# Performance work log

Measured on AMD Instinct MI355X. Metric: run time of the kernel, lower is better.

The kernel has to match this reference:

```python
import jax, jax.numpy as jnp
import numpy as np

B, T, C = 4, 4096, 1024
H = 16          # n_head
LS = 256        # local block size (block-causal window)
EPS = 1e-6


def rmsnorm(x, w):
    # matches RMSNorm: x * rsqrt(mean(x^2) + eps) * weight, computed in fp32
    xf = x.astype(jnp.float32)
    y = xf * jax.lax.rsqrt(jnp.mean(xf * xf, axis=-1, keepdims=True) + EPS)
    return y.astype(x.dtype) * w


def setup_inputs() -> dict:
    key = jax.random.key(0)
    k1, k2, k3 = jax.random.split(key, 3)
    x = jax.random.normal(k1, (B, T, C), dtype=jnp.float32)
    w_qkv = jax.random.normal(k2, (C, 3 * C), dtype=jnp.float32) * (1.0 / np.sqrt(C))
    ln_w = jnp.ones((C,), dtype=jnp.float32)
    w_proj = jax.random.normal(k3, (C, C), dtype=jnp.float32) * (1.0 / np.sqrt(C))
    return {"x": x, "w_qkv": w_qkv, "ln_w": ln_w, "w_proj": w_proj}


def reference(x, w_qkv, ln_w, w_proj):
    Bx, Tx, Cx = x.shape
    ng = Tx // LS                      # number of causal blocks
    hd = Cx // H                       # head dim
    # group tokens into blocks: [B, ng, ls, C]
    xg = x.reshape(Bx, ng, LS, Cx)
    qkv = jnp.einsum('bglc,cd->bgld', xg, w_qkv)
    q, k, v = jnp.split(qkv, 3, axis=-1)
    # fused QK RMSNorm over full embed dim (before head split), shared weight
    q = rmsnorm(q, ln_w)
    k = rmsnorm(k, ln_w)
    # split heads: [B, ng, H, ls, hd]
    q = q.reshape(Bx, ng, LS, H, hd).transpose(0, 1, 3, 2, 4)
    k = k.reshape(Bx, ng, LS, H, hd).transpose(0, 1, 3, 2, 4)
    v = v.reshape(Bx, ng, LS, H, hd).transpose(0, 1, 3, 2, 4)
    scale = 1.0 / np.sqrt(hd)          # muP=False
    att = jnp.einsum('bghqd,bghkd->bghqk', q, k) * scale
    causal = jnp.tril(jnp.ones((LS, LS), dtype=bool))
    att = jnp.where(causal, att, -jnp.finfo(att.dtype).max)
    att = jax.nn.softmax(att, axis=-1)
    y = jnp.einsum('bghqk,bghkd->bghqd', att, v)
    # merge heads and blocks back: [B, T, C]
    y = y.transpose(0, 1, 3, 2, 4).reshape(Bx, Tx, Cx)
    return jnp.einsum('btc,cd->btd', y, w_proj)
```

## Files before the change

### kernel.cpp

```cpp
#include <hip/hip_runtime.h>

typedef __attribute__((ext_vector_type(4))) float f32x4;
typedef __attribute__((ext_vector_type(8))) short bf16x8;
typedef __attribute__((ext_vector_type(4))) unsigned short u16x4;
typedef __attribute__((ext_vector_type(8))) unsigned short u16x8;
typedef unsigned short u16;
typedef unsigned int u32;

#define M_  16384
#define C_  1024
#define N1_ 3072

__device__ __forceinline__ float bf2f(u16 u) {
  union { u32 i; float f; } v; v.i = ((u32)u) << 16; return v.f;
}
__device__ __forceinline__ u16 f2bf(float f) {
  union { float f; u32 i; } v; v.f = f;
  u32 r = v.i + 0x7fffu + ((v.i >> 16) & 1u);
  return (u16)(r >> 16);
}

__device__ __forceinline__ void gload16(const void* g, void* l) {
  __builtin_amdgcn_global_load_lds(
      (const __attribute__((address_space(1))) u32*)g,
      (__attribute__((address_space(3))) u32*)l, 16, 0, 0);
}

__global__ __launch_bounds__(256) void cast_f32_bf16(const float* __restrict__ in,
                                                     u16* __restrict__ out) {
  size_t i = (size_t)blockIdx.x * 256 + threadIdx.x;
  f32x4 v = ((const f32x4*)in)[i];
  u16x4 o = { f2bf(v[0]), f2bf(v[1]), f2bf(v[2]), f2bf(v[3]) };
  ((u16x4*)out)[i] = o;
}

__global__ __launch_bounds__(256) void transpose_cast(const float* __restrict__ in,
                                                      u16* __restrict__ out, int K, int N) {
  __shared__ u16 tile[64][65];
  const int n0 = blockIdx.x * 64, k0 = blockIdx.y * 64;
  const int tid = threadIdx.x;
  const int nn = tid & 63, kk = tid >> 6;
#pragma unroll
  for (int r = 0; r < 16; ++r)
    tile[kk * 16 + r][nn] = f2bf(in[(size_t)(k0 + kk * 16 + r) * N + n0 + nn]);
  __syncthreads();
  const int kc = tid & 15, nl = tid >> 4;
#pragma unroll
  for (int p = 0; p < 4; ++p) {
    const int n = p * 16 + nl;
    u16x4 v = { tile[kc * 4 + 0][n], tile[kc * 4 + 1][n],
                tile[kc * 4 + 2][n], tile[kc * 4 + 3][n] };
    *(u16x4*)(out + (size_t)(n0 + n) * K + k0 + kc * 4) = v;
  }
}

__device__ __forceinline__ void store16(float* dst, f32x4 v0, f32x4 v1, f32x4 v2, f32x4 v3) {
  ((f32x4*)dst)[0] = v0; ((f32x4*)dst)[1] = v1; ((f32x4*)dst)[2] = v2; ((f32x4*)dst)[3] = v3;
}
__device__ __forceinline__ void store16(u16* dst, f32x4 v0, f32x4 v1, f32x4 v2, f32x4 v3) {
  u16x8 o0 = { f2bf(v0[0]), f2bf(v0[1]), f2bf(v0[2]), f2bf(v0[3]),
               f2bf(v1[0]), f2bf(v1[1]), f2bf(v1[2]), f2bf(v1[3]) };
  u16x8 o1 = { f2bf(v2[0]), f2bf(v2[1]), f2bf(v2[2]), f2bf(v2[3]),
               f2bf(v3[0]), f2bf(v3[1]), f2bf(v3[2]), f2bf(v3[3]) };
  *(u16x8*)dst = o0; *(u16x8*)(dst + 8) = o1;
}

template <typename OUT>
__global__ __launch_bounds__(512, 2) void gemm256(const u16* __restrict__ A,
                                                  const u16* __restrict__ BT,
                                                  OUT* __restrict__ C,
                                                  int M, int N, int ntn) {
  constexpr int KC = 1024;
  __shared__ __align__(16) u16 sA0[256 * 64], sA1[256 * 64];
  __shared__ __align__(16) u16 sB0[256 * 64], sB1[256 * 64];
  const int tid = threadIdx.x, lane = tid & 63, w = tid >> 6;
  const int wm = w >> 2, wn = w & 3;

  int bid = blockIdx.x;
  const int cpx = gridDim.x >> 3;
  bid = (bid & 7) * cpx + (bid >> 3);
  const int tm = (bid / ntn) << 8, tn = (bid % ntn) << 8;

  const u16* srcA[4]; const u16* srcB[4]; int ldsOff[4];
#pragma unroll
  for (int l = 0; l < 4; ++l) {
    const int g = l * 512 + tid;
    const int row = g >> 3, c = g & 7;
    srcA[l] = A + (size_t)(tm + row) * KC + ((c ^ (row & 7)) << 3);
    srcB[l] = BT + (size_t)(tn + row) * KC + ((c ^ (row & 7)) << 3);
    ldsOff[l] = g << 4;
  }

#define STAGE(sa, sb, kt) do { const int _k0 = (kt) << 6;                      \
    _Pragma("unroll") for (int _l = 0; _l < 4; ++_l) {                         \
      gload16(srcA[_l] + _k0, (char*)(sa) + ldsOff[_l]);                       \
      gload16(srcB[_l] + _k0, (char*)(sb) + ldsOff[_l]); } } while (0)

  const int swz = (lane & 7) << 4;
  const int r16 = lane & 15;
  const int kb = (lane >> 4) << 4;
#define LDA_(sa, fm, ks) (*(const bf16x8*)((const char*)(sa) + \
    (wm * 128 + (fm) * 16 + r16) * 128 + ((((ks) << 6) | kb) ^ swz)))
#define LDB_(sb, fn, ks) (*(const bf16x8*)((const char*)(sb) + \
    (wn * 64 + (fn) * 16 + r16) * 128 + ((((ks) << 6) | kb) ^ swz)))

  f32x4 acc[8][4];
#pragma unroll
  for (int i = 0; i < 8; ++i)
#pragma unroll
    for (int j = 0; j < 4; ++j) acc[i][j] = (f32x4){0.f, 0.f, 0.f, 0.f};

#define MM(i, j, a_, b_) acc[i][j] = __builtin_amdgcn_mfma_f32_16x16x32_bf16(a_, b_, acc[i][j], 0, 0, 0)

#define KTILE(sa, sb, ...) do {                                                \
  bf16x8 ka[4][2], kb0[2][2], kb1[2][2];                                       \
  _Pragma("unroll") for (int fm = 0; fm < 4; ++fm) {                           \
    ka[fm][0] = LDA_(sa, fm, 0); ka[fm][1] = LDA_(sa, fm, 1); }                \
  _Pragma("unroll") for (int fn = 0; fn < 2; ++fn) {                           \
    kb0[fn][0] = LDB_(sb, fn, 0); kb0[fn][1] = LDB_(sb, fn, 1); }              \
  __builtin_amdgcn_s_barrier();                                                \
  __builtin_amdgcn_s_setprio(1);                                               \
  _Pragma("unroll") for (int fm = 0; fm < 4; ++fm)                             \
    _Pragma("unroll") for (int fn = 0; fn < 2; ++fn) {                         \
      MM(fm, fn, ka[fm][0], kb0[fn][0]); MM(fm, fn, ka[fm][1], kb0[fn][1]); }  \
  __builtin_amdgcn_s_setprio(0);                                               \
  __builtin_amdgcn_s_barrier();                                                \
  _Pragma("unroll") for (int fn = 0; fn < 2; ++fn) {                           \
    kb1[fn][0] = LDB_(sb, 2 + fn, 0); kb1[fn][1] = LDB_(sb, 2 + fn, 1); }      \
  __builtin_amdgcn_s_barrier();                                                \
  __builtin_amdgcn_s_setprio(1);                                               \
  _Pragma("unroll") for (int fm = 0; fm < 4; ++fm)                             \
    _Pragma("unroll") for (int fn = 0; fn < 2; ++fn) {                         \
      MM(fm, 2 + fn, ka[fm][0], kb1[fn][0]); MM(fm, 2 + fn, ka[fm][1], kb1[fn][1]); } \
  __builtin_amdgcn_s_setprio(0);                                               \
  __builtin_amdgcn_s_barrier();                                                \
  _Pragma("unroll") for (int fm = 0; fm < 4; ++fm) {                           \
    ka[fm][0] = LDA_(sa, 4 + fm, 0); ka[fm][1] = LDA_(sa, 4 + fm, 1); }        \
  __builtin_amdgcn_s_barrier();                                                \
  __builtin_amdgcn_s_setprio(1);                                               \
  _Pragma("unroll") for (int fm = 0; fm < 4; ++fm)                             \
    _Pragma("unroll") for (int fn = 0; fn < 2; ++fn) {                         \
      MM(4 + fm, 2 + fn, ka[fm][0], kb1[fn][0]); MM(4 + fm, 2 + fn, ka[fm][1], kb1[fn][1]); } \
  __builtin_amdgcn_s_setprio(0);                                               \
  __builtin_amdgcn_s_barrier();                                                \
  __builtin_amdgcn_sched_barrier(0);                                           \
  __VA_ARGS__;                                                                 \
  __builtin_amdgcn_s_setprio(1);                                               \
  _Pragma("unroll") for (int fm = 0; fm < 4; ++fm)                             \
    _Pragma("unroll") for (int fn = 0; fn < 2; ++fn) {                         \
      MM(4 + fm, fn, ka[fm][0], kb0[fn][0]); MM(4 + fm, fn, ka[fm][1], kb0[fn][1]); } \
  __builtin_amdgcn_s_setprio(0);                                               \
} while (0)

#define TILE_ENTRY(vm) do { __builtin_amdgcn_sched_barrier(0);                 \
    asm volatile("s_waitcnt vmcnt(" #vm ")");                                  \
    __builtin_amdgcn_sched_barrier(0);                                         \
    __builtin_amdgcn_s_barrier();                                              \
    __builtin_amdgcn_sched_barrier(0); } while (0)

  STAGE(sA0, sB0, 0);
  STAGE(sA1, sB1, 1);

#pragma unroll 1
  for (int i = 0; i < 7; ++i) {
    TILE_ENTRY(8);
    KTILE(sA0, sB0, STAGE(sA0, sB0, 2 * i + 2));
    TILE_ENTRY(8);
    KTILE(sA1, sB1, STAGE(sA1, sB1, 2 * i + 3));
  }
  TILE_ENTRY(8);
  KTILE(sA0, sB0, (void)0);
  TILE_ENTRY(0);
  KTILE(sA1, sB1, (void)0);

  __syncthreads();
  u16* eb = (w == 0) ? sA0 : (w == 1) ? sA0 + 8192 : (w == 2) ? sA1 : (w == 3) ? sA1 + 8192
          : (w == 4) ? sB0 : (w == 5) ? sB0 + 8192 : (w == 6) ? sB1 : sB1 + 8192;
  float* fb = (float*)eb;
  const int erow = lane >> 2, eseg = lane & 3;
#pragma unroll
  for (int fm = 0; fm < 8; ++fm) {
#pragma unroll
    for (int fn = 0; fn < 4; ++fn)
#pragma unroll
      for (int r = 0; r < 4; ++r)
        fb[((lane >> 4) * 4 + r) * 68 + fn * 16 + (lane & 15)] = acc[fm][fn][r];
    asm volatile("s_waitcnt lgkmcnt(0)" ::: "memory");
    const float* src = &fb[erow * 68 + eseg * 16];
    f32x4 v0 = ((const f32x4*)src)[0], v1 = ((const f32x4*)src)[1];
    f32x4 v2 = ((const f32x4*)src)[2], v3 = ((const f32x4*)src)[3];
    OUT* dst = C + (size_t)(tm + wm * 128 + fm * 16 + erow) * N + tn + wn * 64 + eseg * 16;
    store16(dst, v0, v1, v2, v3);
  }
#undef STAGE
#undef LDA_
#undef LDB_
#undef MM
#undef KTILE
#undef TILE_ENTRY
}

__global__ __launch_bounds__(256) void qk_scales(const u16* __restrict__ qkv,
                                                 float* __restrict__ qscl,
                                                 float* __restrict__ kscl) {
  const int t = blockIdx.x * 4 + (threadIdx.x >> 6);
  const int lane = threadIdx.x & 63;
  const u16* row = qkv + (size_t)t * N1_;
#pragma unroll
  for (int part = 0; part < 2; ++part) {
    const u16* p = row + part * C_ + lane * 16;
    bf16x8 v0 = *(const bf16x8*)p;
    bf16x8 v1 = *(const bf16x8*)(p + 8);
    float ss = 0.f;
#pragma unroll
    for (int e = 0; e < 8; ++e) {
      float a = bf2f((u16)v0[e]), b = bf2f((u16)v1[e]);
      ss += a * a + b * b;
    }
#pragma unroll
    for (int o = 1; o < 64; o <<= 1) ss += __shfl_xor(ss, o, 64);
    if (lane == 0) {
      float s = rsqrtf(ss * (1.0f / 1024.0f) + 1e-6f);
      (part ? kscl : qscl)[t] = s;
    }
  }
}

__global__ __launch_bounds__(256, 1) void attn_kernel(const u16* __restrict__ qkv,
                                                      const float* __restrict__ qscl,
                                                      const float* __restrict__ kscl,
                                                      const float* __restrict__ lnw,
                                                      u16* __restrict__ y) {
  const int bid = blockIdx.x;
  const int h = bid & 15;
  const int bg = bid >> 4;
  const size_t rowbase = (size_t)bg * 256;
  const u16* Qg = qkv + rowbase * N1_ + h * 64;
  const u16* Kg = Qg + C_;
  const u16* Vg = Qg + 2 * C_;

  __shared__ __align__(16) u16 Ks[256 * 64];
  __shared__ __align__(16) u16 Vt[64 * 256];
  __shared__ __align__(16) u16 Ps[4][16 * 256];

  const int tid = threadIdx.x;
  const int lane = tid & 63;
  const int w = tid >> 6;
  const int g = lane >> 4;
  const int qi = lane & 15;

  {
    const int r = tid;
    const u16* kr = Kg + (size_t)r * N1_;
    const u16* vr = Vg + (size_t)r * N1_;
    const float ksc = kscl[rowbase + r];
    const float* lw = lnw + h * 64;
    char* ksb = (char*)Ks + r * 128;
    const int swk = (r & 7) << 4;
#pragma unroll
    for (int j = 0; j < 8; ++j) {
      bf16x8 kv = *(const bf16x8*)(kr + j * 8);
      f32x4 wa = *(const f32x4*)(lw + j * 8);
      f32x4 wb = *(const f32x4*)(lw + j * 8 + 4);
#pragma unroll
      for (int e = 0; e < 4; ++e) {
        kv[e]     = (short)f2bf(bf2f((u16)kv[e]) * ksc * wa[e]);
        kv[4 + e] = (short)f2bf(bf2f((u16)kv[4 + e]) * ksc * wb[e]);
      }
      *(bf16x8*)(ksb + ((j * 16) ^ swk)) = kv;
      bf16x8 vv = *(const bf16x8*)(vr + j * 8);
#pragma unroll
      for (int e = 0; e < 8; ++e) {
        int d = j * 8 + e;
        *(u16*)((char*)Vt + d * 512 + ((2 * r) ^ ((d & 7) << 4))) = (u16)vv[e];
      }
    }
  }
  float lnq0[8], lnq1[8];
#pragma unroll
  for (int e = 0; e < 8; ++e) {
    lnq0[e] = lnw[h * 64 + g * 8 + e];
    lnq1[e] = lnw[h * 64 + 32 + g * 8 + e];
  }
  __syncthreads();

  const float scale = 0.125f;
  char* pb = (char*)Ps[w];
  const int swq = (qi & 7) << 4;

#pragma unroll 1
  for (int j = 0; j < 4; ++j) {
    const int qt = ((j >> 1) << 3) + ((j & 1) ? (7 - w) : w);

    const u16* qrow = Qg + (size_t)(qt * 16 + qi) * N1_ + g * 8;
    const float qsc = qscl[rowbase + qt * 16 + qi];
    bf16x8 q0 = *(const bf16x8*)(qrow);
    bf16x8 q1 = *(const bf16x8*)(qrow + 32);
#pragma unroll
    for (int e = 0; e < 8; ++e) {
      q0[e] = (short)f2bf(bf2f((u16)q0[e]) * qsc * lnq0[e]);
      q1[e] = (short)f2bf(bf2f((u16)q1[e]) * qsc * lnq1[e]);
    }

    f32x4 s[16];
#pragma unroll
    for (int n = 0; n < 16; ++n) {
      if (n <= qt) {
        const char* kb = (const char*)Ks + (n * 16 + qi) * 128;
        bf16x8 ka0 = *(const bf16x8*)(kb + ((g * 16) ^ swq));
        bf16x8 ka1 = *(const bf16x8*)(kb + ((g * 16 + 64) ^ swq));
        f32x4 a = {0.f, 0.f, 0.f, 0.f};
        a = __builtin_amdgcn_mfma_f32_16x16x32_bf16(ka0, q0, a, 0, 0, 0);
        a = __builtin_amdgcn_mfma_f32_16x16x32_bf16(ka1, q1, a, 0, 0, 0);
        s[n] = a;
      }
    }

    const int q_abs = qt * 16 + qi;
    float m = -3e38f;
#pragma unroll
    for (int n = 0; n < 16; ++n) if (n <= qt) {
#pragma unroll
      for (int r = 0; r < 4; ++r) {
        const int k_abs = n * 16 + g * 4 + r;
        float v = s[n][r] * scale;
        v = (k_abs <= q_abs) ? v : -3e38f;
        s[n][r] = v;
        m = fmaxf(m, v);
      }
    }
    m = fmaxf(m, __shfl_xor(m, 16, 64));
    m = fmaxf(m, __shfl_xor(m, 32, 64));

    float sum = 0.f;
#pragma unroll
    for (int n = 0; n < 16; ++n) if (n <= qt) {
#pragma unroll
      for (int r = 0; r < 4; ++r) {
        float p = __expf(s[n][r] - m);
        s[n][r] = p;
        sum += p;
      }
    }
    sum += __shfl_xor(sum, 16, 64);
    sum += __shfl_xor(sum, 32, 64);

#pragma unroll
    for (int n = 0; n < 16; ++n) if (n <= qt) {
      u16x4 pk = { f2bf(s[n][0]), f2bf(s[n][1]), f2bf(s[n][2]), f2bf(s[n][3]) };
      *(u16x4*)(pb + qi * 512 + ((n * 32 + g * 8) ^ swq)) = pk;
    }
    if (!(qt & 1)) {
      u16x4 z = {0, 0, 0, 0};
      *(u16x4*)(pb + qi * 512 + (((qt + 1) * 32 + g * 8) ^ swq)) = z;
    }

    f32x4 yacc[4];
#pragma unroll
    for (int dn = 0; dn < 4; ++dn) yacc[dn] = (f32x4){0.f, 0.f, 0.f, 0.f};
    const int nkf = qt / 2 + 1;
#pragma unroll
    for (int kf = 0; kf < 8; ++kf) if (kf < nkf) {
      bf16x8 pa = *(const bf16x8*)(pb + qi * 512 + ((kf * 64 + g * 16) ^ swq));
#pragma unroll
      for (int dn = 0; dn < 4; ++dn) {
        const int d = dn * 16 + qi;
        bf16x8 vb = *(const bf16x8*)((const char*)Vt + d * 512 + ((kf * 64 + g * 16) ^ swq));
        yacc[dn] = __builtin_amdgcn_mfma_f32_16x16x32_bf16(pa, vb, yacc[dn], 0, 0, 0);
      }
    }

#pragma unroll
    for (int r = 0; r < 4; ++r) {
      const float inv = 1.0f / __shfl(sum, g * 4 + r, 64);
      const size_t trow = rowbase + (size_t)qt * 16 + g * 4 + r;
      u16* yrow = y + trow * C_ + h * 64 + qi;
#pragma unroll
      for (int dn = 0; dn < 4; ++dn) yrow[dn * 16] = f2bf(yacc[dn][r] * inv);
    }
  }
}

extern "C" void kernel_launch(void* const* d_in, const int* in_sizes, int n_in,
                              void* d_out, int out_size, void* d_ws, size_t ws_size,
                              hipStream_t stream) {
  const float* x      = (const float*)d_in[0];
  const float* w_qkv  = (const float*)d_in[1];
  const float* ln_w   = (const float*)d_in[2];
  const float* w_proj = (const float*)d_in[3];
  float* out = (float*)d_out;

  u16* xb     = (u16*)d_ws;
  u16* wqkvT  = xb + (size_t)M_ * C_;
  u16* wprojT = wqkvT + (size_t)N1_ * C_;
  u16* qkvb   = wprojT + (size_t)C_ * C_;
  u16* yb     = qkvb + (size_t)M_ * N1_;
  float* qscl = (float*)(yb + (size_t)M_ * C_);
  float* kscl = qscl + M_;

  cast_f32_bf16<<<(M_ * C_) / 1024, 256, 0, stream>>>(x, xb);
  transpose_cast<<<dim3(N1_ / 64, C_ / 64), 256, 0, stream>>>(w_qkv, wqkvT, C_, N1_);
  transpose_cast<<<dim3(C_ / 64, C_ / 64), 256, 0, stream>>>(w_proj, wprojT, C_, C_);

  gemm256<u16><<<(M_ / 256) * (N1_ / 256), 512, 0, stream>>>(xb, wqkvT, qkvb, M_, N1_, N1_ / 256);
  qk_scales<<<M_ / 4, 256, 0, stream>>>(qkvb, qscl, kscl);
  attn_kernel<<<64 * 16, 256, 0, stream>>>(qkvb, qscl, kscl, ln_w, yb);
  gemm256<float><<<(M_ / 256) * (C_ / 256), 512, 0, stream>>>(yb, wprojT, out, M_, C_, C_ / 256);
}
```

Before: 293.7 us.

## Fuse QK sum-of-squares into QKV GEMM epilogue and store per-head blocked layout

```diff
diff --git a/kernel.cpp b/kernel.cpp
--- a/kernel.cpp
+++ b/kernel.cpp
@@ -10,6 +10,7 @@
 #define M_  16384
 #define C_  1024
 #define N1_ 3072
+#define PSZ ((size_t)M_ * 64 * 16 / 16 * 4 / 4)
 
 __device__ __forceinline__ float bf2f(u16 u) {
   union { u32 i; float f; } v; v.i = ((u32)u) << 16; return v.f;
@@ -69,10 +70,13 @@
 __global__ __launch_bounds__(512, 2) void gemm256(const u16* __restrict__ A,
                                                   const u16* __restrict__ BT,
                                                   OUT* __restrict__ C,
-                                                  int M, int N, int ntn) {
+                                                  int M, int N, int ntn,
+                                                  float* __restrict__ ssq,
+                                                  float* __restrict__ ssk) {
   constexpr int KC = 1024;
   __shared__ __align__(16) u16 sA0[256 * 64], sA1[256 * 64];
   __shared__ __align__(16) u16 sB0[256 * 64], sB1[256 * 64];
+  __shared__ float ssred[4][256];
   const int tid = threadIdx.x, lane = tid & 63, w = tid >> 6;
   const int wm = w >> 2, wn = w & 3;
 
@@ -174,10 +178,40 @@
   KTILE(sA1, sB1, (void)0);
 
   __syncthreads();
+
+  const int part = tn >> 10;
+  const int cp = tn & 1023;
+  const int bg = tm >> 8;
+  const int hh = (cp >> 6) + wn;
+  if constexpr (sizeof(OUT) == 2) {
+    if (part < 2) {
+#pragma unroll
+      for (int fm = 0; fm < 8; ++fm)
+#pragma unroll
+        for (int r = 0; r < 4; ++r) {
+          float s = acc[fm][0][r] * acc[fm][0][r] + acc[fm][1][r] * acc[fm][1][r]
+                  + acc[fm][2][r] * acc[fm][2][r] + acc[fm][3][r] * acc[fm][3][r];
+          s += __shfl_xor(s, 1, 64); s += __shfl_xor(s, 2, 64);
+          s += __shfl_xor(s, 4, 64); s += __shfl_xor(s, 8, 64);
+          if (r16 == 0) ssred[wn][wm * 128 + fm * 16 + (lane >> 4) * 4 + r] = s;
+        }
+      __syncthreads();
+      if (tid < 256) {
+        float s = ssred[0][tid] + ssred[1][tid] + ssred[2][tid] + ssred[3][tid];
+        (part == 0 ? ssq : ssk)[(size_t)(tm + tid) * 4 + (cp >> 8)] = s;
+      }
+    }
+  }
+
   u16* eb = (w == 0) ? sA0 : (w == 1) ? sA0 + 8192 : (w == 2) ? sA1 : (w == 3) ? sA1 + 8192
           : (w == 4) ? sB0 : (w == 5) ? sB0 + 8192 : (w == 6) ? sB1 : sB1 + 8192;
   float* fb = (float*)eb;
   const int erow = lane >> 2, eseg = lane & 3;
+  OUT* dstb;
+  if constexpr (sizeof(OUT) == 2)
+    dstb = C + (size_t)part * ((size_t)M_ * C_) + ((size_t)(bg * 16 + hh) * 256) * 64;
+  else
+    dstb = C + (size_t)(tm) * N + tn + wn * 64;
 #pragma unroll
   for (int fm = 0; fm < 8; ++fm) {
 #pragma unroll
@@ -189,7 +223,11 @@
     const float* src = &fb[erow * 68 + eseg * 16];
     f32x4 v0 = ((const f32x4*)src)[0], v1 = ((const f32x4*)src)[1];
     f32x4 v2 = ((const f32x4*)src)[2], v3 = ((const f32x4*)src)[3];
-    OUT* dst = C + (size_t)(tm + wm * 128 + fm * 16 + erow) * N + tn + wn * 64 + eseg * 16;
+    OUT* dst;
+    if constexpr (sizeof(OUT) == 2)
+      dst = dstb + (size_t)(wm * 128 + fm * 16 + erow) * 64 + eseg * 16;
+    else
+      dst = dstb + (size_t)(wm * 128 + fm * 16 + erow) * N + eseg * 16;
     store16(dst, v0, v1, v2, v3);
   }
 #undef STAGE
@@ -200,48 +238,22 @@
 #undef TILE_ENTRY
 }
 
-__global__ __launch_bounds__(256) void qk_scales(const u16* __restrict__ qkv,
-                                                 float* __restrict__ qscl,
-                                                 float* __restrict__ kscl) {
-  const int t = blockIdx.x * 4 + (threadIdx.x >> 6);
-  const int lane = threadIdx.x & 63;
-  const u16* row = qkv + (size_t)t * N1_;
-#pragma unroll
-  for (int part = 0; part < 2; ++part) {
-    const u16* p = row + part * C_ + lane * 16;
-    bf16x8 v0 = *(const bf16x8*)p;
-    bf16x8 v1 = *(const bf16x8*)(p + 8);
-    float ss = 0.f;
-#pragma unroll
-    for (int e = 0; e < 8; ++e) {
-      float a = bf2f((u16)v0[e]), b = bf2f((u16)v1[e]);
-      ss += a * a + b * b;
-    }
-#pragma unroll
-    for (int o = 1; o < 64; o <<= 1) ss += __shfl_xor(ss, o, 64);
-    if (lane == 0) {
-      float s = rsqrtf(ss * (1.0f / 1024.0f) + 1e-6f);
-      (part ? kscl : qscl)[t] = s;
-    }
-  }
-}
-
-__global__ __launch_bounds__(256, 1) void attn_kernel(const u16* __restrict__ qkv,
-                                                      const float* __restrict__ qscl,
-                                                      const float* __restrict__ kscl,
+__global__ __launch_bounds__(256, 2) void attn_kernel(const u16* __restrict__ qkvblk,
+                                                      const float* __restrict__ ssq,
+                                                      const float* __restrict__ ssk,
                                                       const float* __restrict__ lnw,
                                                       u16* __restrict__ y) {
   const int bid = blockIdx.x;
   const int h = bid & 15;
   const int bg = bid >> 4;
   const size_t rowbase = (size_t)bg * 256;
-  const u16* Qg = qkv + rowbase * N1_ + h * 64;
-  const u16* Kg = Qg + C_;
-  const u16* Vg = Qg + 2 * C_;
-
-  __shared__ __align__(16) u16 Ks[256 * 64];
+  const u16* Qb = qkvblk + ((size_t)(bg * 16 + h) * 256) * 64;
+  const u16* Kb = Qb + (size_t)M_ * C_;
+  const u16* Vb = Qb + 2 * (size_t)M_ * C_;
+
   __shared__ __align__(16) u16 Vt[64 * 256];
   __shared__ __align__(16) u16 Ps[4][16 * 256];
+  __shared__ float kscl[256];
 
   const int tid = threadIdx.x;
   const int lane = tid & 63;
@@ -251,23 +263,9 @@
 
   {
     const int r = tid;
-    const u16* kr = Kg + (size_t)r * N1_;
-    const u16* vr = Vg + (size_t)r * N1_;
-    const float ksc = kscl[rowbase + r];
-    const float* lw = lnw + h * 64;
-    char* ksb = (char*)Ks + r * 128;
-    const int swk = (r & 7) << 4;
+    const u16* vr = Vb + (size_t)r * 64;
 #pragma unroll
     for (int j = 0; j < 8; ++j) {
-      bf16x8 kv = *(const bf16x8*)(kr + j * 8);
-      f32x4 wa = *(const f32x4*)(lw + j * 8);
-      f32x4 wb = *(const f32x4*)(lw + j * 8 + 4);
-#pragma unroll
-      for (int e = 0; e < 4; ++e) {
-        kv[e]     = (short)f2bf(bf2f((u16)kv[e]) * ksc * wa[e]);
-        kv[4 + e] = (short)f2bf(bf2f((u16)kv[4 + e]) * ksc * wb[e]);
-      }
-      *(bf16x8*)(ksb + ((j * 16) ^ swk)) = kv;
       bf16x8 vv = *(const bf16x8*)(vr + j * 8);
 #pragma unroll
       for (int e = 0; e < 8; ++e) {
@@ -275,25 +273,29 @@
         *(u16*)((char*)Vt + d * 512 + ((2 * r) ^ ((d & 7) << 4))) = (u16)vv[e];
       }
     }
+    f32x4 kp = ((const f32x4*)ssk)[rowbase + r];
+    kscl[r] = rsqrtf((kp[0] + kp[1] + kp[2] + kp[3]) * (1.0f / 1024.0f) + 1e-6f);
   }
   float lnq0[8], lnq1[8];
 #pragma unroll
   for (int e = 0; e < 8; ++e) {
-    lnq0[e] = lnw[h * 64 + g * 8 + e];
-    lnq1[e] = lnw[h * 64 + 32 + g * 8 + e];
+    float a = lnw[h * 64 + g * 8 + e];
+    float b = lnw[h * 64 + 32 + g * 8 + e];
+    lnq0[e] = a * a; lnq1[e] = b * b;
   }
   __syncthreads();
 
-  const float scale = 0.125f;
   char* pb = (char*)Ps[w];
   const int swq = (qi & 7) << 4;
 
 #pragma unroll 1
   for (int j = 0; j < 4; ++j) {
     const int qt = ((j >> 1) << 3) + ((j & 1) ? (7 - w) : w);
-
-    const u16* qrow = Qg + (size_t)(qt * 16 + qi) * N1_ + g * 8;
-    const float qsc = qscl[rowbase + qt * 16 + qi];
+    const int q = qt * 16 + qi;
+
+    f32x4 qv = ((const f32x4*)ssq)[rowbase + q];
+    const float qsc = rsqrtf((qv[0] + qv[1] + qv[2] + qv[3]) * (1.0f / 1024.0f) + 1e-6f);
+    const u16* qrow = Qb + (size_t)q * 64 + g * 8;
     bf16x8 q0 = *(const bf16x8*)(qrow);
     bf16x8 q1 = *(const bf16x8*)(qrow + 32);
 #pragma unroll
@@ -306,9 +308,9 @@
 #pragma unroll
     for (int n = 0; n < 16; ++n) {
       if (n <= qt) {
-        const char* kb = (const char*)Ks + (n * 16 + qi) * 128;
-        bf16x8 ka0 = *(const bf16x8*)(kb + ((g * 16) ^ swq));
-        bf16x8 ka1 = *(const bf16x8*)(kb + ((g * 16 + 64) ^ swq));
+        const u16* krow = Kb + (size_t)(n * 16 + qi) * 64 + g * 8;
+        bf16x8 ka0 = *(const bf16x8*)(krow);
+        bf16x8 ka1 = *(const bf16x8*)(krow + 32);
         f32x4 a = {0.f, 0.f, 0.f, 0.f};
         a = __builtin_amdgcn_mfma_f32_16x16x32_bf16(ka0, q0, a, 0, 0, 0);
         a = __builtin_amdgcn_mfma_f32_16x16x32_bf16(ka1, q1, a, 0, 0, 0);
@@ -316,15 +318,15 @@
       }
     }
 
-    const int q_abs = qt * 16 + qi;
     float m = -3e38f;
 #pragma unroll
     for (int n = 0; n < 16; ++n) if (n <= qt) {
+      f32x4 k4 = *(const f32x4*)&kscl[n * 16 + g * 4];
 #pragma unroll
       for (int r = 0; r < 4; ++r) {
         const int k_abs = n * 16 + g * 4 + r;
-        float v = s[n][r] * scale;
-        v = (k_abs <= q_abs) ? v : -3e38f;
+        float v = s[n][r] * 0.125f * k4[r];
+        v = (k_abs <= q) ? v : -3e38f;
         s[n][r] = v;
         m = fmaxf(m, v);
       }
@@ -393,17 +395,16 @@
   u16* xb     = (u16*)d_ws;
   u16* wqkvT  = xb + (size_t)M_ * C_;
   u16* wprojT = wqkvT + (size_t)N1_ * C_;
-  u16* qkvb   = wprojT + (size_t)C_ * C_;
-  u16* yb     = qkvb + (size_t)M_ * N1_;
-  float* qscl = (float*)(yb + (size_t)M_ * C_);
-  float* kscl = qscl + M_;
+  u16* qkvblk = wprojT + (size_t)C_ * C_;
+  u16* yb     = qkvblk + 3 * (size_t)M_ * C_;
+  float* ssq  = (float*)(yb + (size_t)M_ * C_);
+  float* ssk  = ssq + (size_t)M_ * 4;
 
   cast_f32_bf16<<<(M_ * C_) / 1024, 256, 0, stream>>>(x, xb);
   transpose_cast<<<dim3(N1_ / 64, C_ / 64), 256, 0, stream>>>(w_qkv, wqkvT, C_, N1_);
   transpose_cast<<<dim3(C_ / 64, C_ / 64), 256, 0, stream>>>(w_proj, wprojT, C_, C_);
 
-  gemm256<u16><<<(M_ / 256) * (N1_ / 256), 512, 0, stream>>>(xb, wqkvT, qkvb, M_, N1_, N1_ / 256);
-  qk_scales<<<M_ / 4, 256, 0, stream>>>(qkvb, qscl, kscl);
-  attn_kernel<<<64 * 16, 256, 0, stream>>>(qkvb, qscl, kscl, ln_w, yb);
-  gemm256<float><<<(M_ / 256) * (C_ / 256), 512, 0, stream>>>(yb, wprojT, out, M_, C_, C_ / 256);
-}
+  gemm256<u16><<<(M_ / 256) * (N1_ / 256), 512, 0, stream>>>(xb, wqkvT, qkvblk, M_, N1_, N1_ / 256, ssq, ssk);
+  attn_kernel<<<64 * 16, 256, 0, stream>>>(qkvblk, ssq, ssk, ln_w, yb);
+  gemm256<float><<<(M_ / 256) * (C_ / 256), 512, 0, stream>>>(yb, wprojT, out, M_, C_, C_ / 256, nullptr, nullptr);
+}
```

Measured after the change: 258.5 us. 1.14x faster.
